# Kernel optimization log

Hardware: AMD Instinct MI355X
Metric: run time of the kernel (lower is better)

The kernel has to match this reference:

```python
import jax, jax.numpy as jnp
import numpy as np

B, Q, K, D, H = 4, 2048, 2048, 512, 8
HD = D // H
_INF = -1e30


def setup_inputs() -> dict:
    key = jax.random.key(0)
    ks = jax.random.split(key, 8)
    scale = 1.0 / HD ** 0.5
    return {
        "query": jax.random.normal(ks[0], (B, Q, D), jnp.float32),
        "key": jax.random.normal(ks[1], (B, K, D), jnp.float32),
        "value": jax.random.normal(ks[2], (B, K, D), jnp.float32),
        "Wq": jax.random.normal(ks[3], (D, D), jnp.float32) * scale,  # [out,in]
        "Wk": jax.random.normal(ks[4], (D, D), jnp.float32) * scale,
        "Wv": jax.random.normal(ks[5], (D, D), jnp.float32) * scale,
        "Wo": jax.random.normal(ks[6], (D, D), jnp.float32) * scale,
        "attn_mask": jax.random.randint(ks[7], (B, K), 0, 2, jnp.int32),
    }


def reference(query, key, value, Wq, Wk, Wv, Wo, attn_mask):
    bsz, qlen, _ = query.shape
    klen = key.shape[1]
    head_q = (query @ Wq.T).reshape(bsz, qlen, H, HD)
    head_k = (key @ Wk.T).reshape(bsz, klen, H, HD)
    head_v = (value @ Wv.T).reshape(bsz, klen, H, HD)
    scale = 1.0 / HD ** 0.5
    # [b, i, j, n] score tensor, as in the torch einsum 'bind,bjnd->bijn'
    attn_score = jnp.einsum('bind,bjnd->bijn', head_q, head_k) * scale
    mask = (attn_mask == 0)[:, None, :, None]  # dim-2 mask branch
    attn_score = jnp.where(mask, _INF, attn_score)
    attn_prob = jax.nn.softmax(attn_score, axis=2)  # softmax over key axis j
    attn_vec = jnp.einsum('bijn,bjnd->bind', attn_prob, head_v)
    attn_vec = attn_vec.reshape(bsz, qlen, H * HD)
    return attn_vec @ Wo.T
```

## Files before the change

kernel.cpp:

```cpp
#include <hip/hip_runtime.h>

constexpr int Bc   = 4;
constexpr int Qlen = 2048;
constexpr int Klen = 2048;
constexpr int Dm   = 512;
constexpr int Hh   = 8;
constexpr int HDim = 64;
constexpr float C1 = 0.125f * 1.4426950408889634f;

typedef __attribute__((ext_vector_type(8))) short short8;
typedef __attribute__((ext_vector_type(8))) _Float16 half8;
typedef __attribute__((ext_vector_type(2))) __fp16 fp16x2;
typedef __attribute__((ext_vector_type(4))) float f32x4;

__device__ __forceinline__ f32x4 MFMA16(short8 a, short8 b, f32x4 c) {
  return __builtin_amdgcn_mfma_f32_16x16x32_f16(
      __builtin_bit_cast(half8, a), __builtin_bit_cast(half8, b), c, 0, 0, 0);
}

__device__ __forceinline__ void gload_lds16(const void* g, void* l) {
  __builtin_amdgcn_global_load_lds(
      (const __attribute__((address_space(1))) void*)g,
      (__attribute__((address_space(3))) void*)l, 16, 0, 0);
}

__device__ __forceinline__ unsigned short f2h(float f) {
  _Float16 h = (_Float16)f;
  return __builtin_bit_cast(unsigned short, h);
}

__device__ __forceinline__ unsigned pk2h(float a, float b) {
  fp16x2 h = __builtin_amdgcn_cvt_pkrtz(a, b);
  return __builtin_bit_cast(unsigned, h);
}

__global__ __launch_bounds__(256) void scan_mask(
    const int* __restrict__ msk, int* __restrict__ idx, int* __restrict__ cnt) {
  const int b = blockIdx.x;
  const int tid = threadIdx.x;
  __shared__ int wtot[4];
  const int* mrow = msk + b * Klen;
  int m8[8];
  int c = 0;
#pragma unroll
  for (int i = 0; i < 8; ++i) {
    m8[i] = mrow[tid * 8 + i];
    c += (m8[i] != 0);
  }
  int pre = c;
#pragma unroll
  for (int off = 1; off < 64; off <<= 1) {
    int t = __shfl_up(pre, off);
    if ((tid & 63) >= off) pre += t;
  }
  const int w = tid >> 6;
  if ((tid & 63) == 63) wtot[w] = pre;
  __syncthreads();
  int base = 0;
  for (int i = 0; i < w; ++i) base += wtot[i];
  int p = base + pre - c;
#pragma unroll
  for (int i = 0; i < 8; ++i)
    if (m8[i] != 0) idx[b * Klen + (p++)] = tid * 8 + i;
  if (tid == 255) cnt[b] = base + pre;
}

__global__ __launch_bounds__(256) void cvt4(
    const float* __restrict__ s0, const float* __restrict__ s1,
    const float* __restrict__ s2, const float* __restrict__ s3,
    unsigned short* __restrict__ o0, unsigned short* __restrict__ o1,
    unsigned short* __restrict__ o2, unsigned short* __restrict__ o3,
    const int* __restrict__ msk, float* __restrict__ biasf) {
  const int seg = blockIdx.y;
  int i = (blockIdx.x * 256 + threadIdx.x) * 4;
  if (seg < 4) {
    const float* s = (seg == 0) ? s0 : (seg == 1) ? s1 : (seg == 2) ? s2 : s3;
    unsigned short* o = (seg == 0) ? o0 : (seg == 1) ? o1 : (seg == 2) ? o2 : o3;
    float4 x = *(const float4*)(s + i);
    unsigned t[2] = {pk2h(x.x, x.y), pk2h(x.z, x.w)};
    *(uint2*)(o + i) = *(const uint2*)t;
  } else if (i + 3 < Bc * Klen) {
    int4 m = *(const int4*)(msk + i);
    float4 bo;
    bo.x = (m.x == 0) ? -60000.0f : 0.0f;
    bo.y = (m.y == 0) ? -60000.0f : 0.0f;
    bo.z = (m.z == 0) ? -60000.0f : 0.0f;
    bo.w = (m.w == 0) ? -60000.0f : 0.0f;
    *(float4*)(biasf + i) = bo;
  }
}

__global__ __launch_bounds__(256) void cvt_in(
    const float* __restrict__ q, const float* __restrict__ k,
    const float* __restrict__ v,
    unsigned short* __restrict__ qh, unsigned short* __restrict__ kh,
    unsigned short* __restrict__ vh,
    const int* __restrict__ idx, const int* __restrict__ cnt) {
  const int seg = blockIdx.y;
  int g = blockIdx.x * 256 + threadIdx.x;
  int i = g * 4;
  if (seg == 0) {
    float4 x = *(const float4*)(q + i);
    unsigned t[2] = {pk2h(x.x, x.y), pk2h(x.z, x.w)};
    *(uint2*)(qh + i) = *(const uint2*)t;
    return;
  }
  const float* s = (seg == 1) ? k : v;
  unsigned short* o = (seg == 1) ? kh : vh;
  int row = i >> 9, col = i & 511;
  int b = row >> 11, jc = row & 2047;
  int cb = cnt[b];
  if (jc < cb) {
    int j = idx[b * Klen + jc];
    float4 x = *(const float4*)(s + ((size_t)(b * Klen + j)) * 512 + col);
    unsigned t[2] = {pk2h(x.x, x.y), pk2h(x.z, x.w)};
    *(uint2*)(o + (size_t)row * 512 + col) = *(const uint2*)t;
  } else if (jc < ((cb + 127) & ~127)) {
    uint2 z = {0u, 0u};
    *(uint2*)(o + (size_t)row * 512 + col) = z;
  }
}

template <bool F16A>
__global__ __launch_bounds__(256) void gemm_qkv(
    const float* __restrict__ q_in,
    const float* __restrict__ k_in,
    const float* __restrict__ v_in,
    const unsigned short* __restrict__ qh,
    const unsigned short* __restrict__ kh,
    const unsigned short* __restrict__ vh,
    const unsigned short* __restrict__ Wqh,
    const unsigned short* __restrict__ Wkh,
    const unsigned short* __restrict__ Wvh,
    unsigned short* __restrict__ Qp,
    unsigned short* __restrict__ Kp,
    unsigned short* __restrict__ Vp,
    const int* __restrict__ cnt) {
  __shared__ unsigned short As[128 * 32];
  __shared__ unsigned short Bs[128 * 32];
  const int tid = threadIdx.x;
  const int w = tid >> 6, l = tid & 63;
  const int quad = l >> 4, l15 = l & 15;
  const int m0 = blockIdx.x * 128;
  const int n0 = blockIdx.y * 128;
  const int seg = n0 >> 9;
  const int f0  = n0 & 511;
  if constexpr (F16A) {
    if (seg != 0) {
      int local = m0 & 2047;
      if (local >= ((cnt[m0 >> 11] + 63) & ~63)) return;
    }
  }
  const float* Af = (seg == 0) ? q_in : (seg == 1) ? k_in : v_in;
  const unsigned short* Ah = (seg == 0) ? qh : (seg == 1) ? kh : vh;
  const unsigned short* W = (seg == 0) ? Wqh : (seg == 1) ? Wkh : Wvh;
  unsigned short* dst = (seg == 0) ? Qp : (seg == 1) ? Kp : Vp;

  f32x4 acc[4][4] = {};
  const int lrow = l >> 2;
  const int lcol = (l & 3) * 8;
  const int wm = (w >> 1) * 64, wn = (w & 1) * 64;

  for (int kk = 0; kk < 512; kk += 32) {
#pragma unroll
    for (int i = 0; i < 2; ++i) {
      int row = w * 32 + i * 16 + lrow;
      if constexpr (F16A) {
        gload_lds16(Ah + (size_t)(m0 + row) * 512 + kk + lcol, &As[row * 32 + lcol]);
      } else {
        const float* ap = Af + (size_t)(m0 + row) * 512 + kk + lcol;
        float4 x0 = *(const float4*)(ap);
        float4 x1 = *(const float4*)(ap + 4);
        unsigned t[4] = {pk2h(x0.x, x0.y), pk2h(x0.z, x0.w),
                         pk2h(x1.x, x1.y), pk2h(x1.z, x1.w)};
        *(uint4*)&As[row * 32 + lcol] = *(const uint4*)t;
      }
      gload_lds16(W + (size_t)(f0 + row) * 512 + kk + lcol, &Bs[row * 32 + lcol]);
    }
    __syncthreads();
    short8 af[4], bf[4];
#pragma unroll
    for (int t = 0; t < 4; ++t)
      af[t] = *(const short8*)&As[(wm + t * 16 + l15) * 32 + quad * 8];
#pragma unroll
    for (int t = 0; t < 4; ++t)
      bf[t] = *(const short8*)&Bs[(wn + t * 16 + l15) * 32 + quad * 8];
#pragma unroll
    for (int mt = 0; mt < 4; ++mt)
#pragma unroll
      for (int nt = 0; nt < 4; ++nt)
        acc[mt][nt] = MFMA16(af[mt], bf[nt], acc[mt][nt]);
    __syncthreads();
  }
  const float oscale = (seg == 0) ? C1 : 1.0f;
#pragma unroll
  for (int mt = 0; mt < 4; ++mt)
#pragma unroll
    for (int nt = 0; nt < 4; ++nt)
#pragma unroll
      for (int r = 0; r < 4; ++r) {
        int m  = m0 + wm + mt * 16 + quad * 4 + r;
        int nn = f0 + wn + nt * 16 + l15;
        int b = m >> 11, qq = m & 2047;
        int h = nn >> 6, hd = nn & 63;
        dst[(((size_t)(b * Hh + h)) * Qlen + qq) * HDim + hd] =
            f2h(acc[mt][nt][r] * oscale);
      }
}

__global__ __launch_bounds__(256) void transpose_v(
    const unsigned short* __restrict__ Vp, unsigned short* __restrict__ Vt,
    const int* __restrict__ cnt) {
  __shared__ unsigned short t[64 * 72];
  const int bh = blockIdx.y, jt = blockIdx.x;
  if (cnt) {
    if (jt * 64 >= ((cnt[bh >> 3] + 63) & ~63)) return;
  }
  const int tid = threadIdx.x;
#pragma unroll
  for (int i = 0; i < 2; ++i) {
    int g = i * 256 + tid;
    int j = g >> 3, c8 = g & 7;
    *(uint4*)&t[j * 72 + c8 * 8] =
        *(const uint4*)(Vp + ((size_t)bh * Klen + jt * 64 + j) * 64 + c8 * 8);
  }
  __syncthreads();
#pragma unroll
  for (int i = 0; i < 2; ++i) {
    int g = i * 256 + tid;
    int d = g >> 3, j8 = g & 7;
    unsigned short tmp[8];
#pragma unroll
    for (int kx = 0; kx < 8; ++kx) tmp[kx] = t[(j8 * 8 + kx) * 72 + d];
    *(uint4*)(Vt + ((size_t)bh * HDim + d) * Klen + jt * 64 + j8 * 8) = *(const uint4*)tmp;
  }
}

__global__ __launch_bounds__(256) void gemm_out(
    const unsigned short* __restrict__ Oa,
    const unsigned short* __restrict__ Woh,
    float* __restrict__ out) {
  __shared__ unsigned short As[128 * 32];
  __shared__ unsigned short Bs[128 * 32];
  const int tid = threadIdx.x;
  const int w = tid >> 6, l = tid & 63;
  const int quad = l >> 4, l15 = l & 15;
  const int m0 = blockIdx.x * 128;
  const int n0 = blockIdx.y * 128;

  f32x4 acc[4][4] = {};
  const int lrow = l >> 2;
  const int lcol = (l & 3) * 8;
  const int wm = (w >> 1) * 64, wn = (w & 1) * 64;

  for (int kk = 0; kk < 512; kk += 32) {
#pragma unroll
    for (int i = 0; i < 2; ++i) {
      int row = w * 32 + i * 16 + lrow;
      gload_lds16(Oa + (size_t)(m0 + row) * 512 + kk + lcol, &As[row * 32 + lcol]);
      gload_lds16(Woh + (size_t)(n0 + row) * 512 + kk + lcol, &Bs[row * 32 + lcol]);
    }
    __syncthreads();
    short8 af[4], bf[4];
#pragma unroll
    for (int t = 0; t < 4; ++t)
      af[t] = *(const short8*)&As[(wm + t * 16 + l15) * 32 + quad * 8];
#pragma unroll
    for (int t = 0; t < 4; ++t)
      bf[t] = *(const short8*)&Bs[(wn + t * 16 + l15) * 32 + quad * 8];
#pragma unroll
    for (int mt = 0; mt < 4; ++mt)
#pragma unroll
      for (int nt = 0; nt < 4; ++nt)
        acc[mt][nt] = MFMA16(af[mt], bf[nt], acc[mt][nt]);
    __syncthreads();
  }
#pragma unroll
  for (int mt = 0; mt < 4; ++mt)
#pragma unroll
    for (int nt = 0; nt < 4; ++nt)
#pragma unroll
      for (int r = 0; r < 4; ++r) {
        int m  = m0 + wm + mt * 16 + quad * 4 + r;
        int nn = n0 + wn + nt * 16 + l15;
        out[(size_t)m * 512 + nn] = acc[mt][nt][r];
      }
}

template <bool KSPLIT, bool COMPACT>
__global__ __launch_bounds__(256, 4) void attn(
    const unsigned short* __restrict__ Qp,
    const unsigned short* __restrict__ Kp,
    const unsigned short* __restrict__ Vt,
    const float* __restrict__ biasf,
    const int* __restrict__ cntArr,
    unsigned short* __restrict__ Oa,
    unsigned short* __restrict__ Op,
    float* __restrict__ Sp) {
  __shared__ unsigned short Ks[64 * 64];
  __shared__ unsigned short Vs[64 * 64];
  __shared__ unsigned short Ps[4][16 * 72];

  const int tid = threadIdx.x;
  const int w = tid >> 6, l = tid & 63;
  const int quad = l >> 4, l15 = l & 15;
  const int bid = blockIdx.x;
  const int bh = bid & 31;
  const int b = bh >> 3, h = bh & 7;

  int cnt, KT;
  if constexpr (COMPACT) {
    cnt = cntArr[b];
    KT = (cnt + 63) >> 6;
  } else {
    cnt = Klen;
    KT = Klen / 64;
  }

  int qt, part, kt0, ktN;
  if constexpr (KSPLIT) {
    int rest = bid >> 5;
    part = rest & 1;
    qt = rest >> 1;
    int half = (KT + 1) >> 1;
    kt0 = part ? half : 0;
    ktN = part ? KT : half;
  } else {
    part = 0; qt = bid >> 5; kt0 = 0; ktN = KT;
  }
  const int x = l15 & 7;
  const int qrow = qt * 64 + w * 16 + l15;

  short8 aq[2];
#pragma unroll
  for (int k2 = 0; k2 < 2; ++k2)
    aq[k2] = *(const short8*)(Qp + ((size_t)bh * Qlen + qrow) * HDim + (k2 * 4 + quad) * 8);

  short8 ones;
#pragma unroll
  for (int j = 0; j < 8; ++j) ones[j] = (short)0x3C00;

  f32x4 o[4] = {};
  f32x4 o5 = {};
  float m_run = -1.0e6f;
  const float* brow = biasf + b * Klen;

  for (int kt = kt0; kt < ktN; ++kt) {
    __syncthreads();
#pragma unroll
    for (int i = 0; i < 2; ++i) {
      int g = i * 256 + tid;
      int row = g >> 3, c8 = g & 7;
      int sb = (c8 ^ (row & 7)) * 8;
      gload_lds16(Kp + ((size_t)bh * Klen + kt * 64 + row) * HDim + sb, &Ks[g * 8]);
      gload_lds16(Vt + ((size_t)bh * HDim + row) * Klen + kt * 64 + sb, &Vs[g * 8]);
    }
    float4 bb[4];
    if constexpr (!COMPACT) {
#pragma unroll
      for (int ct = 0; ct < 4; ++ct)
        bb[ct] = *(const float4*)(brow + kt * 64 + ct * 16 + quad * 4);
    }
    __syncthreads();

    f32x4 sv[4];
#pragma unroll
    for (int ct = 0; ct < 4; ++ct) {
      const short8 bk0 = *(const short8*)&Ks[(ct * 16 + l15) * 64 + (quad ^ x) * 8];
      const short8 bk1 = *(const short8*)&Ks[(ct * 16 + l15) * 64 + ((4 + quad) ^ x) * 8];
      f32x4 a = {};
      a = MFMA16(bk0, aq[0], a);
      a = MFMA16(bk1, aq[1], a);
      sv[ct] = a;
    }

    if constexpr (!COMPACT) {
#pragma unroll
      for (int ct = 0; ct < 4; ++ct)
#pragma unroll
        for (int r = 0; r < 4; ++r)
          sv[ct][r] += bb[ct][r];
    } else {
      if (kt == KT - 1) {
#pragma unroll
        for (int ct = 0; ct < 4; ++ct)
#pragma unroll
          for (int r = 0; r < 4; ++r)
            if (kt * 64 + ct * 16 + quad * 4 + r >= cnt) sv[ct][r] = -60000.0f;
      }
    }

    float mx0 = fmaxf(fmaxf(sv[0][0], sv[0][1]), fmaxf(sv[0][2], sv[0][3]));
    float mx1 = fmaxf(fmaxf(sv[1][0], sv[1][1]), fmaxf(sv[1][2], sv[1][3]));
    float mx2 = fmaxf(fmaxf(sv[2][0], sv[2][1]), fmaxf(sv[2][2], sv[2][3]));
    float mx3 = fmaxf(fmaxf(sv[3][0], sv[3][1]), fmaxf(sv[3][2], sv[3][3]));
    float mx = fmaxf(fmaxf(mx0, mx1), fmaxf(mx2, mx3));
    mx = fmaxf(mx, __shfl_xor(mx, 16));
    mx = fmaxf(mx, __shfl_xor(mx, 32));
    if (__any(mx > m_run + 8.0f)) {
      float mnew  = fmaxf(m_run, mx);
      float alpha = exp2f(m_run - mnew);
      m_run = mnew;
#pragma unroll
      for (int ctd = 0; ctd < 4; ++ctd) o[ctd] *= alpha;
      o5 *= alpha;
    }

#pragma unroll
    for (int ct = 0; ct < 4; ++ct) {
      float p0 = exp2f(sv[ct][0] - m_run);
      float p1 = exp2f(sv[ct][1] - m_run);
      float p2 = exp2f(sv[ct][2] - m_run);
      float p3 = exp2f(sv[ct][3] - m_run);
      unsigned pk[2] = {pk2h(p0, p1), pk2h(p2, p3)};
      *(uint2*)&Ps[w][l15 * 72 + ct * 16 + quad * 4] = *(const uint2*)pk;
    }
    const short8 ap0 = *(const short8*)&Ps[w][l15 * 72 + quad * 8];
    const short8 ap1 = *(const short8*)&Ps[w][l15 * 72 + 32 + quad * 8];

    o5 = MFMA16(ones, ap0, o5);
    o5 = MFMA16(ones, ap1, o5);

#pragma unroll
    for (int ctd = 0; ctd < 4; ++ctd) {
      const short8 bv0 = *(const short8*)&Vs[(ctd * 16 + l15) * 64 + (quad ^ x) * 8];
      const short8 bv1 = *(const short8*)&Vs[(ctd * 16 + l15) * 64 + ((4 + quad) ^ x) * 8];
      o[ctd] = MFMA16(bv0, ap0, o[ctd]);
      o[ctd] = MFMA16(bv1, ap1, o[ctd]);
    }
  }

  float lt = o5[0];
  float rl = (lt > 0.0f) ? 1.0f / lt : 0.0f;
  if constexpr (KSPLIT) {
    const size_t pbase = ((size_t)part * 32 + bh) * Qlen;
    const size_t obase = (pbase + qrow) * 64;
#pragma unroll
    for (int ctd = 0; ctd < 4; ++ctd) {
      unsigned pk[2] = {pk2h(o[ctd][0] * rl, o[ctd][1] * rl),
                        pk2h(o[ctd][2] * rl, o[ctd][3] * rl)};
      *(uint2*)(Op + obase + ctd * 16 + quad * 4) = *(const uint2*)pk;
    }
    if (l < 16)
      Sp[pbase + qrow] = (lt > 0.0f) ? m_run + log2f(lt) : -1.0e30f;
  } else {
    const size_t obase = ((size_t)(b * Qlen) + qrow) * Dm + h * 64;
#pragma unroll
    for (int ctd = 0; ctd < 4; ++ctd) {
      unsigned pk[2] = {pk2h(o[ctd][0] * rl, o[ctd][1] * rl),
                        pk2h(o[ctd][2] * rl, o[ctd][3] * rl)};
      *(uint2*)(Oa + obase + ctd * 16 + quad * 4) = *(const uint2*)pk;
    }
  }
}

__global__ __launch_bounds__(256) void reduce_o(
    const unsigned short* __restrict__ Op, const float* __restrict__ Sp,
    unsigned short* __restrict__ Oa) {
  int g = blockIdx.x * 256 + threadIdx.x;
  int row = g >> 3, c8 = g & 7;
  const size_t PART = (size_t)32 * Qlen;
  float s1 = Sp[row], s2 = Sp[PART + row];
  float M = fmaxf(s1, s2);
  float w1 = exp2f(s1 - M), w2 = exp2f(s2 - M);
  float rs = 1.0f / (w1 + w2);
  w1 *= rs; w2 *= rs;
  short8 a = *(const short8*)(Op + (size_t)row * 64 + c8 * 8);
  short8 bvec = *(const short8*)(Op + (PART + row) * 64 + c8 * 8);
  half8 af = __builtin_bit_cast(half8, a);
  half8 bf = __builtin_bit_cast(half8, bvec);
  unsigned pk[4];
#pragma unroll
  for (int i = 0; i < 4; ++i) {
    float r0 = w1 * (float)af[i * 2 + 0] + w2 * (float)bf[i * 2 + 0];
    float r1 = w1 * (float)af[i * 2 + 1] + w2 * (float)bf[i * 2 + 1];
    pk[i] = pk2h(r0, r1);
  }
  int bh = row >> 11, qrow = row & 2047;
  int b = bh >> 3, h = bh & 7;
  *(uint4*)(Oa + ((size_t)(b * Qlen) + qrow) * Dm + h * 64 + c8 * 8) =
      *(const uint4*)pk;
}

extern "C" void kernel_launch(void* const* d_in, const int* in_sizes, int n_in,
                              void* d_out, int out_size, void* d_ws, size_t ws_size,
                              hipStream_t stream) {
  const float* q  = (const float*)d_in[0];
  const float* k  = (const float*)d_in[1];
  const float* v  = (const float*)d_in[2];
  const float* Wq = (const float*)d_in[3];
  const float* Wk = (const float*)d_in[4];
  const float* Wv = (const float*)d_in[5];
  const float* Wo = (const float*)d_in[6];
  const int*  msk = (const int*)d_in[7];
  float* out = (float*)d_out;

  char* ws = (char*)d_ws;
  const size_t SEG  = (size_t)Bc * Hh * Qlen * HDim * sizeof(unsigned short);
  const size_t WSEG = (size_t)Dm * Dm * sizeof(unsigned short);
  unsigned short* Qp  = (unsigned short*)(ws);
  unsigned short* Kp  = (unsigned short*)(ws + SEG);
  unsigned short* Vp  = (unsigned short*)(ws + 2 * SEG);
  unsigned short* Vt  = (unsigned short*)(ws + 3 * SEG);
  unsigned short* Oa  = Vp;
  unsigned short* Wqh = (unsigned short*)(ws + 4 * SEG);
  unsigned short* Wkh = (unsigned short*)(ws + 4 * SEG + WSEG);
  unsigned short* Wvh = (unsigned short*)(ws + 4 * SEG + 2 * WSEG);
  unsigned short* Woh = (unsigned short*)(ws + 4 * SEG + 3 * WSEG);
  int*   idxArr = (int*)(ws + 4 * SEG + 4 * WSEG);
  int*   cntArr = idxArr + Bc * Klen;
  float* Bfs    = (float*)idxArr;
  unsigned short* qh  = (unsigned short*)(ws + 4 * SEG + 4 * WSEG + 65536);
  unsigned short* kh  = qh + SEG / 2;
  unsigned short* vh  = kh + SEG / 2;
  unsigned short* Op  = qh;
  float*          Sp  = (float*)vh;
  const size_t NEED = 4 * SEG + 4 * WSEG + 65536 + 3 * SEG;
  const bool big = ws_size >= NEED;

  auto attn_split  = attn<true, true>;
  auto attn_single = attn<false, false>;

  const int wn = Dm * Dm;
  if (big) {
    hipLaunchKernelGGL(scan_mask, dim3(Bc), dim3(256), 0, stream, msk, idxArr, cntArr);
    hipLaunchKernelGGL(cvt4, dim3(wn / 1024, 4), dim3(256), 0, stream,
                       Wq, Wk, Wv, Wo, Wqh, Wkh, Wvh, Woh, msk, Bfs);
    hipLaunchKernelGGL(cvt_in, dim3(4096, 3), dim3(256), 0, stream,
                       q, k, v, qh, kh, vh, idxArr, cntArr);
    hipLaunchKernelGGL(gemm_qkv<true>, dim3(64, 12), dim3(256), 0, stream,
                       q, k, v, qh, kh, vh, Wqh, Wkh, Wvh, Qp, Kp, Vp, cntArr);
    hipLaunchKernelGGL(transpose_v, dim3(32, 32), dim3(256), 0, stream, Vp, Vt, cntArr);
    hipLaunchKernelGGL(attn_split, dim3(2048), dim3(256), 0, stream,
                       Qp, Kp, Vt, Bfs, cntArr, Oa, Op, Sp);
    hipLaunchKernelGGL(reduce_o, dim3(2048), dim3(256), 0, stream, Op, Sp, Oa);
  } else {
    hipLaunchKernelGGL(cvt4, dim3(wn / 1024, 5), dim3(256), 0, stream,
                       Wq, Wk, Wv, Wo, Wqh, Wkh, Wvh, Woh, msk, Bfs);
    hipLaunchKernelGGL(gemm_qkv<false>, dim3(64, 12), dim3(256), 0, stream,
                       q, k, v, qh, kh, vh, Wqh, Wkh, Wvh, Qp, Kp, Vp, cntArr);
    hipLaunchKernelGGL(transpose_v, dim3(32, 32), dim3(256), 0, stream, Vp, Vt,
                       (const int*)nullptr);
    hipLaunchKernelGGL(attn_single, dim3(1024), dim3(256), 0, stream,
                       Qp, Kp, Vt, Bfs, (const int*)nullptr, Oa, Op, Sp);
  }
  hipLaunchKernelGGL(gemm_out, dim3(64, 4), dim3(256), 0, stream, Oa, Woh, out);
}
```

Baseline: 194.1 us.

## Double-buffer LDS tiles in GEMM and attention kernels, add MFMA priority hints

The QKV projection, output projection and attention kernels now keep two LDS buffers per operand. The next K-step or key tile is prefetched into the idle buffer while the current one feeds MFMA, which leaves one barrier per iteration instead of two. The attention loop also raises wave priority around its MFMA sections with s_setprio. This aims to hide global-to-LDS load latency behind matrix math, at the cost of doubled LDS use. In the attention kernel that extra LDS may lower the number of resident blocks per CU below the launch-bounds target.

```diff
diff --git a/kernel.cpp b/kernel.cpp
--- a/kernel.cpp
+++ b/kernel.cpp
@@ -136,8 +136,8 @@
     unsigned short* __restrict__ Kp,
     unsigned short* __restrict__ Vp,
     const int* __restrict__ cnt) {
-  __shared__ unsigned short As[128 * 32];
-  __shared__ unsigned short Bs[128 * 32];
+  __shared__ unsigned short As[2][128 * 32];
+  __shared__ unsigned short Bs[2][128 * 32];
   const int tid = threadIdx.x;
   const int w = tid >> 6, l = tid & 63;
   const int quad = l >> 4, l15 = l & 15;
@@ -161,36 +161,41 @@
   const int lcol = (l & 3) * 8;
   const int wm = (w >> 1) * 64, wn = (w & 1) * 64;
 
-  for (int kk = 0; kk < 512; kk += 32) {
+  auto stage = [&](int bs, int kk) {
 #pragma unroll
     for (int i = 0; i < 2; ++i) {
       int row = w * 32 + i * 16 + lrow;
       if constexpr (F16A) {
-        gload_lds16(Ah + (size_t)(m0 + row) * 512 + kk + lcol, &As[row * 32 + lcol]);
+        gload_lds16(Ah + (size_t)(m0 + row) * 512 + kk + lcol, &As[bs][row * 32 + lcol]);
       } else {
         const float* ap = Af + (size_t)(m0 + row) * 512 + kk + lcol;
         float4 x0 = *(const float4*)(ap);
         float4 x1 = *(const float4*)(ap + 4);
         unsigned t[4] = {pk2h(x0.x, x0.y), pk2h(x0.z, x0.w),
                          pk2h(x1.x, x1.y), pk2h(x1.z, x1.w)};
-        *(uint4*)&As[row * 32 + lcol] = *(const uint4*)t;
+        *(uint4*)&As[bs][row * 32 + lcol] = *(const uint4*)t;
       }
-      gload_lds16(W + (size_t)(f0 + row) * 512 + kk + lcol, &Bs[row * 32 + lcol]);
-    }
+      gload_lds16(W + (size_t)(f0 + row) * 512 + kk + lcol, &Bs[bs][row * 32 + lcol]);
+    }
+  };
+
+  stage(0, 0);
+  for (int kk = 0; kk < 512; kk += 32) {
+    const int cur = (kk >> 5) & 1;
     __syncthreads();
+    if (kk + 32 < 512) stage(cur ^ 1, kk + 32);
     short8 af[4], bf[4];
 #pragma unroll
     for (int t = 0; t < 4; ++t)
-      af[t] = *(const short8*)&As[(wm + t * 16 + l15) * 32 + quad * 8];
+      af[t] = *(const short8*)&As[cur][(wm + t * 16 + l15) * 32 + quad * 8];
 #pragma unroll
     for (int t = 0; t < 4; ++t)
-      bf[t] = *(const short8*)&Bs[(wn + t * 16 + l15) * 32 + quad * 8];
+      bf[t] = *(const short8*)&Bs[cur][(wn + t * 16 + l15) * 32 + quad * 8];
 #pragma unroll
     for (int mt = 0; mt < 4; ++mt)
 #pragma unroll
       for (int nt = 0; nt < 4; ++nt)
         acc[mt][nt] = MFMA16(af[mt], bf[nt], acc[mt][nt]);
-    __syncthreads();
   }
   const float oscale = (seg == 0) ? C1 : 1.0f;
 #pragma unroll
@@ -240,8 +245,8 @@
     const unsigned short* __restrict__ Oa,
     const unsigned short* __restrict__ Woh,
     float* __restrict__ out) {
-  __shared__ unsigned short As[128 * 32];
-  __shared__ unsigned short Bs[128 * 32];
+  __shared__ unsigned short As[2][128 * 32];
+  __shared__ unsigned short Bs[2][128 * 32];
   const int tid = threadIdx.x;
   const int w = tid >> 6, l = tid & 63;
   const int quad = l >> 4, l15 = l & 15;
@@ -253,27 +258,32 @@
   const int lcol = (l & 3) * 8;
   const int wm = (w >> 1) * 64, wn = (w & 1) * 64;
 
-  for (int kk = 0; kk < 512; kk += 32) {
+  auto stage = [&](int bs, int kk) {
 #pragma unroll
     for (int i = 0; i < 2; ++i) {
       int row = w * 32 + i * 16 + lrow;
-      gload_lds16(Oa + (size_t)(m0 + row) * 512 + kk + lcol, &As[row * 32 + lcol]);
-      gload_lds16(Woh + (size_t)(n0 + row) * 512 + kk + lcol, &Bs[row * 32 + lcol]);
-    }
+      gload_lds16(Oa + (size_t)(m0 + row) * 512 + kk + lcol, &As[bs][row * 32 + lcol]);
+      gload_lds16(Woh + (size_t)(n0 + row) * 512 + kk + lcol, &Bs[bs][row * 32 + lcol]);
+    }
+  };
+
+  stage(0, 0);
+  for (int kk = 0; kk < 512; kk += 32) {
+    const int cur = (kk >> 5) & 1;
     __syncthreads();
+    if (kk + 32 < 512) stage(cur ^ 1, kk + 32);
     short8 af[4], bf[4];
 #pragma unroll
     for (int t = 0; t < 4; ++t)
-      af[t] = *(const short8*)&As[(wm + t * 16 + l15) * 32 + quad * 8];
+      af[t] = *(const short8*)&As[cur][(wm + t * 16 + l15) * 32 + quad * 8];
 #pragma unroll
     for (int t = 0; t < 4; ++t)
-      bf[t] = *(const short8*)&Bs[(wn + t * 16 + l15) * 32 + quad * 8];
+      bf[t] = *(const short8*)&Bs[cur][(wn + t * 16 + l15) * 32 + quad * 8];
 #pragma unroll
     for (int mt = 0; mt < 4; ++mt)
 #pragma unroll
       for (int nt = 0; nt < 4; ++nt)
         acc[mt][nt] = MFMA16(af[mt], bf[nt], acc[mt][nt]);
-    __syncthreads();
   }
 #pragma unroll
   for (int mt = 0; mt < 4; ++mt)
@@ -297,8 +307,8 @@
     unsigned short* __restrict__ Oa,
     unsigned short* __restrict__ Op,
     float* __restrict__ Sp) {
-  __shared__ unsigned short Ks[64 * 64];
-  __shared__ unsigned short Vs[64 * 64];
+  __shared__ unsigned short Ks[2][64 * 64];
+  __shared__ unsigned short Vs[2][64 * 64];
   __shared__ unsigned short Ps[4][16 * 72];
 
   const int tid = threadIdx.x;
@@ -345,34 +355,42 @@
   float m_run = -1.0e6f;
   const float* brow = biasf + b * Klen;
 
-  for (int kt = kt0; kt < ktN; ++kt) {
-    __syncthreads();
+  auto stage = [&](int bs, int kt) {
 #pragma unroll
     for (int i = 0; i < 2; ++i) {
       int g = i * 256 + tid;
       int row = g >> 3, c8 = g & 7;
       int sb = (c8 ^ (row & 7)) * 8;
-      gload_lds16(Kp + ((size_t)bh * Klen + kt * 64 + row) * HDim + sb, &Ks[g * 8]);
-      gload_lds16(Vt + ((size_t)bh * HDim + row) * Klen + kt * 64 + sb, &Vs[g * 8]);
-    }
+      gload_lds16(Kp + ((size_t)bh * Klen + kt * 64 + row) * HDim + sb, &Ks[bs][g * 8]);
+      gload_lds16(Vt + ((size_t)bh * HDim + row) * Klen + kt * 64 + sb, &Vs[bs][g * 8]);
+    }
+  };
+
+  stage(0, kt0);
+  for (int kt = kt0; kt < ktN; ++kt) {
+    const int cur = (kt - kt0) & 1;
+    __syncthreads();
+    if (kt + 1 < ktN) stage(cur ^ 1, kt + 1);
+
     float4 bb[4];
     if constexpr (!COMPACT) {
 #pragma unroll
       for (int ct = 0; ct < 4; ++ct)
         bb[ct] = *(const float4*)(brow + kt * 64 + ct * 16 + quad * 4);
     }
-    __syncthreads();
 
     f32x4 sv[4];
+    __builtin_amdgcn_s_setprio(1);
 #pragma unroll
     for (int ct = 0; ct < 4; ++ct) {
-      const short8 bk0 = *(const short8*)&Ks[(ct * 16 + l15) * 64 + (quad ^ x) * 8];
-      const short8 bk1 = *(const short8*)&Ks[(ct * 16 + l15) * 64 + ((4 + quad) ^ x) * 8];
+      const short8 bk0 = *(const short8*)&Ks[cur][(ct * 16 + l15) * 64 + (quad ^ x) * 8];
+      const short8 bk1 = *(const short8*)&Ks[cur][(ct * 16 + l15) * 64 + ((4 + quad) ^ x) * 8];
       f32x4 a = {};
       a = MFMA16(bk0, aq[0], a);
       a = MFMA16(bk1, aq[1], a);
       sv[ct] = a;
     }
+    __builtin_amdgcn_s_setprio(0);
 
     if constexpr (!COMPACT) {
 #pragma unroll
@@ -418,16 +436,17 @@
     const short8 ap0 = *(const short8*)&Ps[w][l15 * 72 + quad * 8];
     const short8 ap1 = *(const short8*)&Ps[w][l15 * 72 + 32 + quad * 8];
 
+    __builtin_amdgcn_s_setprio(1);
     o5 = MFMA16(ones, ap0, o5);
     o5 = MFMA16(ones, ap1, o5);
-
 #pragma unroll
     for (int ctd = 0; ctd < 4; ++ctd) {
-      const short8 bv0 = *(const short8*)&Vs[(ctd * 16 + l15) * 64 + (quad ^ x) * 8];
-      const short8 bv1 = *(const short8*)&Vs[(ctd * 16 + l15) * 64 + ((4 + quad) ^ x) * 8];
+      const short8 bv0 = *(const short8*)&Vs[cur][(ctd * 16 + l15) * 64 + (quad ^ x) * 8];
+      const short8 bv1 = *(const short8*)&Vs[cur][(ctd * 16 + l15) * 64 + ((4 + quad) ^ x) * 8];
       o[ctd] = MFMA16(bv0, ap0, o[ctd]);
       o[ctd] = MFMA16(bv1, ap1, o[ctd]);
     }
+    __builtin_amdgcn_s_setprio(0);
   }
 
   float lt = o5[0];
```

Result: no change. 197.5 us (+1.7%).
